# Kernel tuning notes

Hardware: AMD Instinct MI355X
Metric: run time of the kernel (lower is better)

The kernel has to match this reference:

```python
import jax, jax.numpy as jnp
import numpy as np

DIM = 64
N_EMBED = 1024
B, H, W = 64, 32, 32


def setup_inputs() -> dict:
    key = jax.random.key(0)
    k1, k2 = jax.random.split(key)
    inp = jax.random.normal(k1, (B, H, W, DIM), dtype=jnp.float32)
    embed = jax.random.normal(k2, (DIM, N_EMBED), dtype=jnp.float32)
    return {"input": inp, "embed": embed}


def reference(input, embed):
    # Eval-mode forward of Quantize (EMA buffer updates only run in training).
    dim, n_embed = embed.shape
    flat = input.reshape(-1, dim)  # [N, dim]
    dist = (jnp.sum(flat * flat, axis=1, keepdims=True)
            - 2.0 * (flat @ embed)
            + jnp.sum(embed * embed, axis=0, keepdims=True))
    embed_ind_flat = jnp.argmax(-dist, axis=1)  # nearest code per vector
    quantize_hard = jnp.take(embed.T, embed_ind_flat, axis=0).reshape(input.shape)
    # Soft (softmax-weighted) combine over the codebook
    quant = jax.nn.softmax(-dist, axis=-1) @ embed.T  # [N, dim]
    quant = quant.reshape(input.shape)
    embed_ind = embed_ind_flat.reshape(input.shape[:-1])
    diff = jnp.mean((jax.lax.stop_gradient(quantize_hard) - input) ** 2)
    # Straight-through: forward value = hard codes, gradient flows via soft quant
    quantize = quant + jax.lax.stop_gradient(quantize_hard - quant)
    embed_loss = jnp.mean((quantize - jax.lax.stop_gradient(input)) ** 2)
    return quantize, embed_ind, diff, embed_loss
```

## Files before the change

kernel.cpp:

```cpp
#include <hip/hip_runtime.h>
#include <math.h>

typedef __attribute__((ext_vector_type(8))) short short8;
typedef __attribute__((ext_vector_type(4))) float f32x4;
typedef unsigned short ushort_t;
typedef unsigned int uint_t;

#define DIM 64
#define NE 1024
#define NROW 65536
#define NELEM (NROW * DIM)
#define MARGIN 0.02f

#define OFF_BPACK 0
#define OFF_CN 262144
#define OFF_ET 266240
#define OFF_ACC 528384
#define OFF_FCNT 529408
#define OFF_DONE 529412
#define OFF_FLAGS 529424

__device__ __forceinline__ ushort_t f2bf(float f) {
  uint_t u = __float_as_uint(f);
  uint_t r = (u + 0x7FFFu + ((u >> 16) & 1u)) >> 16;
  return (ushort_t)r;
}

__global__ void prepack_kernel(const float* __restrict__ embed, ushort_t* __restrict__ bp,
                               float* __restrict__ cn, float* __restrict__ et,
                               double* __restrict__ acc, int* __restrict__ fcnt,
                               int* __restrict__ done) {
  __shared__ float nsum[8][32];
  const int tid = threadIdx.x;
  if (blockIdx.x == 0) {
    if (tid < 8) acc[tid * 16] = 0.0;
    if (tid == 0) {
      fcnt[0] = 0;
      done[0] = 0;
    }
  }
  const int cl_ = tid & 31;
  const int dg = tid >> 5;
  const int code = blockIdx.x * 32 + cl_;
  const int c16 = code >> 4, cl = code & 15;
  const int lane = cl + (dg & 3) * 16;
  const int kk = dg >> 2;

  float vals[8];
  float nrm = 0.f;
#pragma unroll
  for (int jd = 0; jd < 8; ++jd) {
    int d = dg * 8 + jd;
    float e = embed[d * NE + code];
    vals[jd] = e;
    nrm = fmaf(e, e, nrm);
  }
  nsum[dg][cl_] = nrm;

  float4 a = {vals[0], vals[1], vals[2], vals[3]};
  float4 b4 = {vals[4], vals[5], vals[6], vals[7]};
  *reinterpret_cast<float4*>(&et[(size_t)code * 64 + dg * 8]) = a;
  *reinterpret_cast<float4*>(&et[(size_t)code * 64 + dg * 8 + 4]) = b4;

  short8 hv, lv;
#pragma unroll
  for (int jd = 0; jd < 8; ++jd) {
    ushort_t h = f2bf(vals[jd]);
    float hf = __uint_as_float((uint_t)h << 16);
    hv[jd] = (short)h;
    lv[jd] = (short)f2bf(vals[jd] - hf);
  }
  *reinterpret_cast<short8*>(&bp[((size_t)(c16 * 4 + kk) * 64 + lane) * 8]) = hv;
  *reinterpret_cast<short8*>(&bp[((size_t)(c16 * 4 + 2 + kk) * 64 + lane) * 8]) = lv;

  __syncthreads();
  if (tid < 32) {
    float s = 0.f;
#pragma unroll
    for (int w = 0; w < 8; ++w) s += nsum[w][tid];
    cn[blockIdx.x * 32 + tid] = s;
  }
}

__launch_bounds__(64, 2)
__global__ void score_kernel(const float* __restrict__ input, const ushort_t* __restrict__ bp,
                             const float* __restrict__ cn, const float* __restrict__ et,
                             float* __restrict__ out, double* __restrict__ acc,
                             int* __restrict__ fcnt, int* __restrict__ flags) {
  __shared__ float cns[NE];
  const int lane = threadIdx.x;
  const int col = lane & 15, g = lane >> 4;
  const long rowbase = (long)blockIdx.x * 32;

#pragma unroll
  for (int i = 0; i < 4; ++i) {
    int o = i * 256 + lane * 4;
    *reinterpret_cast<float4*>(&cns[o]) = *reinterpret_cast<const float4*>(&cn[o]);
  }

  short8 ah[2][2], al[2][2];
#pragma unroll
  for (int rt = 0; rt < 2; ++rt)
#pragma unroll
    for (int kk = 0; kk < 2; ++kk) {
      const float* xp = &input[(size_t)(rowbase + rt * 16 + col) * 64 + kk * 32 + g * 8];
      float4 x0 = *reinterpret_cast<const float4*>(xp);
      float4 x1 = *reinterpret_cast<const float4*>(xp + 4);
      float xs[8] = {x0.x, x0.y, x0.z, x0.w, x1.x, x1.y, x1.z, x1.w};
#pragma unroll
      for (int j = 0; j < 8; ++j) {
        ushort_t h = f2bf(xs[j]);
        ah[rt][kk][j] = (short)h;
        float hf = __uint_as_float((uint_t)h << 16);
        al[rt][kk][j] = (short)f2bf(xs[j] - hf);
      }
    }

  float v1[2][4], v2[2][4];
  int i1[2][4];
#pragma unroll
  for (int rt = 0; rt < 2; ++rt)
#pragma unroll
    for (int r = 0; r < 4; ++r) {
      v1[rt][r] = -INFINITY;
      v2[rt][r] = -INFINITY;
      i1[rt][r] = 0;
    }

  __syncthreads();

  const short8* bpv = reinterpret_cast<const short8*>(bp);

  short8 b0h0, b0h1, b0l0, b0l1, b1h0, b1h1, b1l0, b1l1;
#define LOADB(B, cc)                       \
  {                                        \
    b##B##h0 = bpv[(cc)*256 + lane];       \
    b##B##h1 = bpv[(cc)*256 + 64 + lane];  \
    b##B##l0 = bpv[(cc)*256 + 128 + lane]; \
    b##B##l1 = bpv[(cc)*256 + 192 + lane]; \
  }

#define COMPUTE(B, cc)                                                            \
  {                                                                               \
    float cnv = cns[(cc)*16 + col];                                               \
    f32x4 aA = {0.f, 0.f, 0.f, 0.f};                                              \
    f32x4 aB = {0.f, 0.f, 0.f, 0.f};                                              \
    aA = __builtin_amdgcn_mfma_f32_16x16x32_bf16(ah[0][0], b##B##h0, aA, 0, 0, 0); \
    aB = __builtin_amdgcn_mfma_f32_16x16x32_bf16(ah[1][0], b##B##h0, aB, 0, 0, 0); \
    aA = __builtin_amdgcn_mfma_f32_16x16x32_bf16(ah[0][1], b##B##h1, aA, 0, 0, 0); \
    aB = __builtin_amdgcn_mfma_f32_16x16x32_bf16(ah[1][1], b##B##h1, aB, 0, 0, 0); \
    aA = __builtin_amdgcn_mfma_f32_16x16x32_bf16(al[0][0], b##B##h0, aA, 0, 0, 0); \
    aB = __builtin_amdgcn_mfma_f32_16x16x32_bf16(al[1][0], b##B##h0, aB, 0, 0, 0); \
    aA = __builtin_amdgcn_mfma_f32_16x16x32_bf16(al[0][1], b##B##h1, aA, 0, 0, 0); \
    aB = __builtin_amdgcn_mfma_f32_16x16x32_bf16(al[1][1], b##B##h1, aB, 0, 0, 0); \
    aA = __builtin_amdgcn_mfma_f32_16x16x32_bf16(ah[0][0], b##B##l0, aA, 0, 0, 0); \
    aB = __builtin_amdgcn_mfma_f32_16x16x32_bf16(ah[1][0], b##B##l0, aB, 0, 0, 0); \
    aA = __builtin_amdgcn_mfma_f32_16x16x32_bf16(ah[0][1], b##B##l1, aA, 0, 0, 0); \
    aB = __builtin_amdgcn_mfma_f32_16x16x32_bf16(ah[1][1], b##B##l1, aB, 0, 0, 0); \
    aA = __builtin_amdgcn_mfma_f32_16x16x32_bf16(al[0][0], b##B##l0, aA, 0, 0, 0); \
    aB = __builtin_amdgcn_mfma_f32_16x16x32_bf16(al[1][0], b##B##l0, aB, 0, 0, 0); \
    aA = __builtin_amdgcn_mfma_f32_16x16x32_bf16(al[0][1], b##B##l1, aA, 0, 0, 0); \
    aB = __builtin_amdgcn_mfma_f32_16x16x32_bf16(al[1][1], b##B##l1, aB, 0, 0, 0); \
    const int code = (cc)*16 + col;                                               \
    _Pragma("unroll") for (int r = 0; r < 4; ++r) {                               \
      float v = fmaf(2.f, aA[r], -cnv);                                           \
      v2[0][r] = __builtin_amdgcn_fmed3f(v, v1[0][r], v2[0][r]);                  \
      bool gt = v > v1[0][r];                                                     \
      i1[0][r] = gt ? code : i1[0][r];                                            \
      v1[0][r] = fmaxf(v1[0][r], v);                                              \
    }                                                                             \
    _Pragma("unroll") for (int r = 0; r < 4; ++r) {                               \
      float v = fmaf(2.f, aB[r], -cnv);                                           \
      v2[1][r] = __builtin_amdgcn_fmed3f(v, v1[1][r], v2[1][r]);                  \
      bool gt = v > v1[1][r];                                                     \
      i1[1][r] = gt ? code : i1[1][r];                                            \
      v1[1][r] = fmaxf(v1[1][r], v);                                              \
    }                                                                             \
  }

  LOADB(0, 0);
  LOADB(1, 1);
#pragma unroll 1
  for (int c = 0; c < 64; c += 2) {
    COMPUTE(0, c);
    if (c + 2 < 64) LOADB(0, c + 2);
    COMPUTE(1, c + 1);
    if (c + 3 < 64) LOADB(1, c + 3);
  }
#undef LOADB
#undef COMPUTE

  double lsum = 0.0;
#pragma unroll
  for (int rt = 0; rt < 2; ++rt)
#pragma unroll
    for (int r = 0; r < 4; ++r) {
      float bv1 = v1[rt][r], bv2 = v2[rt][r];
      int bidx = i1[rt][r];
#pragma unroll
      for (int off = 1; off <= 8; off <<= 1) {
        float ov1 = __shfl_xor(bv1, off);
        int oi = __shfl_xor(bidx, off);
        float ov2 = __shfl_xor(bv2, off);
        bool take = (ov1 > bv1) || (ov1 == bv1 && oi < bidx);
        float nv2 = take ? fmaxf(bv1, ov2) : fmaxf(bv2, ov1);
        bv1 = take ? ov1 : bv1;
        bidx = take ? oi : bidx;
        bv2 = nv2;
      }
      long row = rowbase + rt * 16 + g * 4 + r;
      float4 h = *reinterpret_cast<const float4*>(&et[(size_t)bidx * 64 + col * 4]);
      float4 x = *reinterpret_cast<const float4*>(&input[(size_t)row * 64 + col * 4]);
      *reinterpret_cast<float4*>(&out[(size_t)row * 64 + col * 4]) = h;
      float d0 = h.x - x.x, d1 = h.y - x.y, d2 = h.z - x.z, d3 = h.w - x.w;
      lsum += (double)(d0 * d0 + d1 * d1 + d2 * d2 + d3 * d3);
      if (col == 0) {
        out[NELEM + row] = (float)bidx;
        if (bv1 - bv2 < MARGIN) {
          int p = atomicAdd(fcnt, 1);
          flags[p] = (int)row;
        }
      }
    }

#pragma unroll
  for (int off = 1; off <= 32; off <<= 1) lsum += __shfl_xor(lsum, off);
  if (lane == 0) unsafeAtomicAdd(&acc[(blockIdx.x & 7) * 16], lsum);
}

__global__ void fixup_kernel(const float* __restrict__ input, const float* __restrict__ embed,
                             const float* __restrict__ et, float* __restrict__ out,
                             double* __restrict__ acc, const int* __restrict__ fcnt,
                             const int* __restrict__ flags, int* __restrict__ done) {
  __shared__ float Xs[8][64];
  __shared__ double Wv[4][8];
  __shared__ int Wi[4][8];
  __shared__ int NewI[8], OldI[8], Rw[8];
  const int tid = threadIdx.x;
  const int lane = tid & 63, wv = tid >> 6;
  const int count = *fcnt;

  for (int base = blockIdx.x * 8; base < count; base += gridDim.x * 8) {
    __syncthreads();
    if (tid < 8) {
      int p = base + tid;
      int r = (p < count) ? flags[p] : flags[count - 1];
      Rw[tid] = r;
      OldI[tid] = (int)out[NELEM + r];
    }
    __syncthreads();
    if (tid < 128) {
      int r8 = tid >> 4, seg = (tid & 15) * 4;
      *reinterpret_cast<float4*>(&Xs[r8][seg]) =
          *reinterpret_cast<const float4*>(&input[(size_t)Rw[r8] * 64 + seg]);
    }
    __syncthreads();

    const int j0 = tid * 4;
    double dot[8][4];
    double nrm[4];
#pragma unroll
    for (int r = 0; r < 8; ++r)
#pragma unroll
      for (int cc = 0; cc < 4; ++cc) dot[r][cc] = 0.0;
#pragma unroll
    for (int cc = 0; cc < 4; ++cc) nrm[cc] = 0.0;

#pragma unroll 1
    for (int d = 0; d < 64; d += 4) {
      float4 e4[4];
#pragma unroll
      for (int q = 0; q < 4; ++q)
        e4[q] = *reinterpret_cast<const float4*>(&embed[(d + q) * NE + j0]);
#pragma unroll
      for (int q = 0; q < 4; ++q) {
        double ev[4] = {(double)e4[q].x, (double)e4[q].y, (double)e4[q].z, (double)e4[q].w};
#pragma unroll
        for (int cc = 0; cc < 4; ++cc) nrm[cc] = fma(ev[cc], ev[cc], nrm[cc]);
#pragma unroll
        for (int r = 0; r < 8; ++r) {
          double xr = (double)Xs[r][d + q];
#pragma unroll
          for (int cc = 0; cc < 4; ++cc) dot[r][cc] = fma(xr, ev[cc], dot[r][cc]);
        }
      }
    }

#pragma unroll
    for (int r = 0; r < 8; ++r) {
      double bv = -1e300;
      int bi = 0;
#pragma unroll
      for (int cc = 0; cc < 4; ++cc) {
        double t = 2.0 * dot[r][cc] - nrm[cc];
        if (t > bv) {
          bv = t;
          bi = j0 + cc;
        }
      }
#pragma unroll
      for (int off = 1; off <= 32; off <<= 1) {
        double ob = __shfl_xor(bv, off);
        int oi = __shfl_xor(bi, off);
        if (ob > bv || (ob == bv && oi < bi)) {
          bv = ob;
          bi = oi;
        }
      }
      if (lane == 0) {
        Wv[wv][r] = bv;
        Wi[wv][r] = bi;
      }
    }
    __syncthreads();
    if (tid < 8) {
      double bv = Wv[0][tid];
      int bi = Wi[0][tid];
#pragma unroll
      for (int w = 1; w < 4; ++w) {
        double ob = Wv[w][tid];
        int oi = Wi[w][tid];
        if (ob > bv || (ob == bv && oi < bi)) {
          bv = ob;
          bi = oi;
        }
      }
      NewI[tid] = bi;
      if (base + tid < count && bi != OldI[tid]) out[NELEM + Rw[tid]] = (float)bi;
    }
    __syncthreads();
    if (tid < 128) {
      int r8 = tid >> 4, seg = (tid & 15) * 4;
      if (base + r8 < count && NewI[r8] != OldI[r8]) {
        float4 hn = *reinterpret_cast<const float4*>(&et[(size_t)NewI[r8] * 64 + seg]);
        float4 ho = *reinterpret_cast<const float4*>(&et[(size_t)OldI[r8] * 64 + seg]);
        float4 x = *reinterpret_cast<const float4*>(&Xs[r8][seg]);
        *reinterpret_cast<float4*>(&out[(size_t)Rw[r8] * 64 + seg]) = hn;
        float n0 = hn.x - x.x, n1 = hn.y - x.y, n2 = hn.z - x.z, n3 = hn.w - x.w;
        float o0 = ho.x - x.x, o1 = ho.y - x.y, o2 = ho.z - x.z, o3 = ho.w - x.w;
        double delta = (double)(n0 * n0 + n1 * n1 + n2 * n2 + n3 * n3) -
                       (double)(o0 * o0 + o1 * o1 + o2 * o2 + o3 * o3);
        unsafeAtomicAdd(&acc[(blockIdx.x & 7) * 16], delta);
      }
    }
  }

  __syncthreads();
  if (tid == 0) {
    __threadfence();
    int prev = atomicAdd(done, 1);
    if (prev == (int)gridDim.x - 1) {
      double v = 0.0;
#pragma unroll
      for (int w = 0; w < 8; ++w) v += unsafeAtomicAdd(&acc[w * 16], 0.0);
      float f = (float)(v / (double)NELEM);
      out[NELEM + NROW + 0] = f;
      out[NELEM + NROW + 1] = f;
    }
  }
}

extern "C" void kernel_launch(void* const* d_in, const int* in_sizes, int n_in,
                              void* d_out, int out_size, void* d_ws, size_t ws_size,
                              hipStream_t stream) {
  const float* input = (const float*)d_in[0];
  const float* embed = (const float*)d_in[1];
  float* out = (float*)d_out;
  char* ws = (char*)d_ws;
  ushort_t* bp = (ushort_t*)(ws + OFF_BPACK);
  float* cn = (float*)(ws + OFF_CN);
  float* et = (float*)(ws + OFF_ET);
  double* acc = (double*)(ws + OFF_ACC);
  int* fcnt = (int*)(ws + OFF_FCNT);
  int* done = (int*)(ws + OFF_DONE);
  int* flags = (int*)(ws + OFF_FLAGS);

  prepack_kernel<<<32, 256, 0, stream>>>(embed, bp, cn, et, acc, fcnt, done);
  score_kernel<<<NROW / 32, 64, 0, stream>>>(input, bp, cn, et, out, acc, fcnt, flags);
  fixup_kernel<<<256, 256, 0, stream>>>(input, embed, et, out, acc, fcnt, flags, done);
}
```

Measured before the change: 138.3 us.

## Fuse fixup pass into score kernel and drop low-low MFMA term

Removes the separate fixup kernel. Rows whose top-two score margin is small are now rechecked in double precision inside the score kernel, using a wave-wide ballot loop over a transposed codebook copy. The MFMA product drops the lo*lo bf16 term, uses two independent accumulator chains, and triple-buffers the codebook loads. The prepack kernel is reshaped to 64-thread blocks that reduce norms with shuffles. This removes a kernel launch and the global flag list, at the cost of serialized double-precision work in blocks that contain ambiguous rows.

```diff
diff --git a/kernel.cpp b/kernel.cpp
--- a/kernel.cpp
+++ b/kernel.cpp
@@ -2,6 +2,7 @@
 #include <math.h>
 
 typedef __attribute__((ext_vector_type(8))) short short8;
+typedef __attribute__((ext_vector_type(4))) short short4v;
 typedef __attribute__((ext_vector_type(4))) float f32x4;
 typedef unsigned short ushort_t;
 typedef unsigned int uint_t;
@@ -11,14 +12,13 @@
 #define NROW 65536
 #define NELEM (NROW * DIM)
 #define MARGIN 0.02f
+#define NBLK 2048
 
 #define OFF_BPACK 0
 #define OFF_CN 262144
 #define OFF_ET 266240
 #define OFF_ACC 528384
-#define OFF_FCNT 529408
-#define OFF_DONE 529412
-#define OFF_FLAGS 529424
+#define OFF_DONE 529408
 
 __device__ __forceinline__ ushort_t f2bf(float f) {
   uint_t u = __float_as_uint(f);
@@ -28,66 +28,52 @@
 
 __global__ void prepack_kernel(const float* __restrict__ embed, ushort_t* __restrict__ bp,
                                float* __restrict__ cn, float* __restrict__ et,
-                               double* __restrict__ acc, int* __restrict__ fcnt,
-                               int* __restrict__ done) {
-  __shared__ float nsum[8][32];
-  const int tid = threadIdx.x;
-  if (blockIdx.x == 0) {
-    if (tid < 8) acc[tid * 16] = 0.0;
-    if (tid == 0) {
-      fcnt[0] = 0;
-      done[0] = 0;
-    }
-  }
-  const int cl_ = tid & 31;
-  const int dg = tid >> 5;
-  const int code = blockIdx.x * 32 + cl_;
+                               double* __restrict__ acc, int* __restrict__ done) {
+  const int lane = threadIdx.x;
+  const int blk = blockIdx.x;
+  if (blk == 0) {
+    if (lane < 8) acc[lane * 16] = 0.0;
+    if (lane == 8) done[0] = 0;
+  }
+  const int code = blk * 4 + (lane >> 4);
+  const int dg = lane & 15;
+  const int d0 = dg * 4;
+  float e[4];
+  float nrm = 0.f;
+#pragma unroll
+  for (int q = 0; q < 4; ++q) {
+    e[q] = embed[(d0 + q) * NE + code];
+    nrm = fmaf(e[q], e[q], nrm);
+  }
+  float4 ev = {e[0], e[1], e[2], e[3]};
+  *reinterpret_cast<float4*>(&et[(size_t)code * 64 + d0]) = ev;
+
+  short4v hv, lv;
+#pragma unroll
+  for (int q = 0; q < 4; ++q) {
+    ushort_t h = f2bf(e[q]);
+    float hf = __uint_as_float((uint_t)h << 16);
+    hv[q] = (short)h;
+    lv[q] = (short)f2bf(e[q] - hf);
+  }
   const int c16 = code >> 4, cl = code & 15;
-  const int lane = cl + (dg & 3) * 16;
-  const int kk = dg >> 2;
-
-  float vals[8];
-  float nrm = 0.f;
-#pragma unroll
-  for (int jd = 0; jd < 8; ++jd) {
-    int d = dg * 8 + jd;
-    float e = embed[d * NE + code];
-    vals[jd] = e;
-    nrm = fmaf(e, e, nrm);
-  }
-  nsum[dg][cl_] = nrm;
-
-  float4 a = {vals[0], vals[1], vals[2], vals[3]};
-  float4 b4 = {vals[4], vals[5], vals[6], vals[7]};
-  *reinterpret_cast<float4*>(&et[(size_t)code * 64 + dg * 8]) = a;
-  *reinterpret_cast<float4*>(&et[(size_t)code * 64 + dg * 8 + 4]) = b4;
-
-  short8 hv, lv;
-#pragma unroll
-  for (int jd = 0; jd < 8; ++jd) {
-    ushort_t h = f2bf(vals[jd]);
-    float hf = __uint_as_float((uint_t)h << 16);
-    hv[jd] = (short)h;
-    lv[jd] = (short)f2bf(vals[jd] - hf);
-  }
-  *reinterpret_cast<short8*>(&bp[((size_t)(c16 * 4 + kk) * 64 + lane) * 8]) = hv;
-  *reinterpret_cast<short8*>(&bp[((size_t)(c16 * 4 + 2 + kk) * 64 + lane) * 8]) = lv;
-
-  __syncthreads();
-  if (tid < 32) {
-    float s = 0.f;
-#pragma unroll
-    for (int w = 0; w < 8; ++w) s += nsum[w][tid];
-    cn[blockIdx.x * 32 + tid] = s;
-  }
+  const int lane16 = cl + ((d0 >> 3) & 3) * 16;
+  const int kk = d0 >> 5;
+  const int j0 = d0 & 7;
+  *reinterpret_cast<short4v*>(&bp[((size_t)(c16 * 4 + kk) * 64 + lane16) * 8 + j0]) = hv;
+  *reinterpret_cast<short4v*>(&bp[((size_t)(c16 * 4 + 2 + kk) * 64 + lane16) * 8 + j0]) = lv;
+
+#pragma unroll
+  for (int off = 1; off <= 8; off <<= 1) nrm += __shfl_xor(nrm, off);
+  if (dg == 0) cn[code] = nrm;
 }
 
 __launch_bounds__(64, 2)
 __global__ void score_kernel(const float* __restrict__ input, const ushort_t* __restrict__ bp,
                              const float* __restrict__ cn, const float* __restrict__ et,
                              float* __restrict__ out, double* __restrict__ acc,
-                             int* __restrict__ fcnt, int* __restrict__ flags) {
-  __shared__ float cns[NE];
+                             int* __restrict__ done) {
+  __shared__ __align__(16) float cns[NE];
   const int lane = threadIdx.x;
   const int col = lane & 15, g = lane >> 4;
   const long rowbase = (long)blockIdx.x * 32;
@@ -130,8 +116,8 @@
   __syncthreads();
 
   const short8* bpv = reinterpret_cast<const short8*>(bp);
-
-  short8 b0h0, b0h1, b0l0, b0l1, b1h0, b1h1, b1l0, b1l1;
+  short8 b0h0, b0h1, b0l0, b0l1, b1h0, b1h1, b1l0, b1l1, b2h0, b2h1, b2l0, b2l1;
+
 #define LOADB(B, cc)                       \
   {                                        \
     b##B##h0 = bpv[(cc)*256 + lane];       \
@@ -140,57 +126,58 @@
     b##B##l1 = bpv[(cc)*256 + 192 + lane]; \
   }
 
-#define COMPUTE(B, cc)                                                            \
-  {                                                                               \
-    float cnv = cns[(cc)*16 + col];                                               \
-    f32x4 aA = {0.f, 0.f, 0.f, 0.f};                                              \
-    f32x4 aB = {0.f, 0.f, 0.f, 0.f};                                              \
-    aA = __builtin_amdgcn_mfma_f32_16x16x32_bf16(ah[0][0], b##B##h0, aA, 0, 0, 0); \
-    aB = __builtin_amdgcn_mfma_f32_16x16x32_bf16(ah[1][0], b##B##h0, aB, 0, 0, 0); \
-    aA = __builtin_amdgcn_mfma_f32_16x16x32_bf16(ah[0][1], b##B##h1, aA, 0, 0, 0); \
-    aB = __builtin_amdgcn_mfma_f32_16x16x32_bf16(ah[1][1], b##B##h1, aB, 0, 0, 0); \
-    aA = __builtin_amdgcn_mfma_f32_16x16x32_bf16(al[0][0], b##B##h0, aA, 0, 0, 0); \
-    aB = __builtin_amdgcn_mfma_f32_16x16x32_bf16(al[1][0], b##B##h0, aB, 0, 0, 0); \
-    aA = __builtin_amdgcn_mfma_f32_16x16x32_bf16(al[0][1], b##B##h1, aA, 0, 0, 0); \
-    aB = __builtin_amdgcn_mfma_f32_16x16x32_bf16(al[1][1], b##B##h1, aB, 0, 0, 0); \
-    aA = __builtin_amdgcn_mfma_f32_16x16x32_bf16(ah[0][0], b##B##l0, aA, 0, 0, 0); \
-    aB = __builtin_amdgcn_mfma_f32_16x16x32_bf16(ah[1][0], b##B##l0, aB, 0, 0, 0); \
-    aA = __builtin_amdgcn_mfma_f32_16x16x32_bf16(ah[0][1], b##B##l1, aA, 0, 0, 0); \
-    aB = __builtin_amdgcn_mfma_f32_16x16x32_bf16(ah[1][1], b##B##l1, aB, 0, 0, 0); \
-    aA = __builtin_amdgcn_mfma_f32_16x16x32_bf16(al[0][0], b##B##l0, aA, 0, 0, 0); \
-    aB = __builtin_amdgcn_mfma_f32_16x16x32_bf16(al[1][0], b##B##l0, aB, 0, 0, 0); \
-    aA = __builtin_amdgcn_mfma_f32_16x16x32_bf16(al[0][1], b##B##l1, aA, 0, 0, 0); \
-    aB = __builtin_amdgcn_mfma_f32_16x16x32_bf16(al[1][1], b##B##l1, aB, 0, 0, 0); \
-    const int code = (cc)*16 + col;                                               \
-    _Pragma("unroll") for (int r = 0; r < 4; ++r) {                               \
-      float v = fmaf(2.f, aA[r], -cnv);                                           \
-      v2[0][r] = __builtin_amdgcn_fmed3f(v, v1[0][r], v2[0][r]);                  \
-      bool gt = v > v1[0][r];                                                     \
-      i1[0][r] = gt ? code : i1[0][r];                                            \
-      v1[0][r] = fmaxf(v1[0][r], v);                                              \
-    }                                                                             \
-    _Pragma("unroll") for (int r = 0; r < 4; ++r) {                               \
-      float v = fmaf(2.f, aB[r], -cnv);                                           \
-      v2[1][r] = __builtin_amdgcn_fmed3f(v, v1[1][r], v2[1][r]);                  \
-      bool gt = v > v1[1][r];                                                     \
-      i1[1][r] = gt ? code : i1[1][r];                                            \
-      v1[1][r] = fmaxf(v1[1][r], v);                                              \
-    }                                                                             \
+#define COMPUTE(B, cc)                                                             \
+  {                                                                                \
+    float cnv = cns[(cc)*16 + col];                                                \
+    f32x4 uA = {0.f, 0.f, 0.f, 0.f};                                               \
+    f32x4 uB = {0.f, 0.f, 0.f, 0.f};                                               \
+    f32x4 vA = {0.f, 0.f, 0.f, 0.f};                                               \
+    f32x4 vB = {0.f, 0.f, 0.f, 0.f};                                               \
+    uA = __builtin_amdgcn_mfma_f32_16x16x32_bf16(ah[0][0], b##B##h0, uA, 0, 0, 0); \
+    uB = __builtin_amdgcn_mfma_f32_16x16x32_bf16(ah[1][0], b##B##h0, uB, 0, 0, 0); \
+    vA = __builtin_amdgcn_mfma_f32_16x16x32_bf16(ah[0][0], b##B##l0, vA, 0, 0, 0); \
+    vB = __builtin_amdgcn_mfma_f32_16x16x32_bf16(ah[1][0], b##B##l0, vB, 0, 0, 0); \
+    uA = __builtin_amdgcn_mfma_f32_16x16x32_bf16(ah[0][1], b##B##h1, uA, 0, 0, 0); \
+    uB = __builtin_amdgcn_mfma_f32_16x16x32_bf16(ah[1][1], b##B##h1, uB, 0, 0, 0); \
+    vA = __builtin_amdgcn_mfma_f32_16x16x32_bf16(ah[0][1], b##B##l1, vA, 0, 0, 0); \
+    vB = __builtin_amdgcn_mfma_f32_16x16x32_bf16(ah[1][1], b##B##l1, vB, 0, 0, 0); \
+    vA = __builtin_amdgcn_mfma_f32_16x16x32_bf16(al[0][0], b##B##h0, vA, 0, 0, 0); \
+    vB = __builtin_amdgcn_mfma_f32_16x16x32_bf16(al[1][0], b##B##h0, vB, 0, 0, 0); \
+    vA = __builtin_amdgcn_mfma_f32_16x16x32_bf16(al[0][1], b##B##h1, vA, 0, 0, 0); \
+    vB = __builtin_amdgcn_mfma_f32_16x16x32_bf16(al[1][1], b##B##h1, vB, 0, 0, 0); \
+    const int code = (cc)*16 + col;                                                \
+    _Pragma("unroll") for (int r = 0; r < 4; ++r) {                                \
+      float v = fmaf(2.f, uA[r] + vA[r], -cnv);                                    \
+      v2[0][r] = __builtin_amdgcn_fmed3f(v, v1[0][r], v2[0][r]);                   \
+      bool gt = v > v1[0][r];                                                      \
+      i1[0][r] = gt ? code : i1[0][r];                                             \
+      v1[0][r] = fmaxf(v1[0][r], v);                                               \
+    }                                                                              \
+    _Pragma("unroll") for (int r = 0; r < 4; ++r) {                                \
+      float v = fmaf(2.f, uB[r] + vB[r], -cnv);                                    \
+      v2[1][r] = __builtin_amdgcn_fmed3f(v, v1[1][r], v2[1][r]);                   \
+      bool gt = v > v1[1][r];                                                      \
+      i1[1][r] = gt ? code : i1[1][r];                                             \
+      v1[1][r] = fmaxf(v1[1][r], v);                                               \
+    }                                                                              \
   }
 
   LOADB(0, 0);
   LOADB(1, 1);
+  LOADB(2, 2);
 #pragma unroll 1
-  for (int c = 0; c < 64; c += 2) {
+  for (int c = 0; c < 63; c += 3) {
     COMPUTE(0, c);
-    if (c + 2 < 64) LOADB(0, c + 2);
+    if (c + 3 < 64) LOADB(0, c + 3);
     COMPUTE(1, c + 1);
-    if (c + 3 < 64) LOADB(1, c + 3);
-  }
+    if (c + 4 < 64) LOADB(1, c + 4);
+    COMPUTE(2, c + 2);
+    if (c + 5 < 64) LOADB(2, c + 5);
+  }
+  COMPUTE(0, 63);
 #undef LOADB
 #undef COMPUTE
 
-  double lsum = 0.0;
 #pragma unroll
   for (int rt = 0; rt < 2; ++rt)
 #pragma unroll
@@ -208,148 +195,85 @@
         bidx = take ? oi : bidx;
         bv2 = nv2;
       }
-      long row = rowbase + rt * 16 + g * 4 + r;
+      v1[rt][r] = bv1;
+      v2[rt][r] = bv2;
+      i1[rt][r] = bidx;
+    }
+
+#pragma unroll
+  for (int rt = 0; rt < 2; ++rt)
+#pragma unroll
+    for (int r = 0; r < 4; ++r) {
+      unsigned long long m = __ballot(col == 0 && (v1[rt][r] - v2[rt][r] < MARGIN));
+      while (m) {
+        int p = __ffsll((unsigned long long)m) - 1;
+        m &= m - 1;
+        const int gg = p >> 4;
+        const long row = rowbase + rt * 16 + gg * 4 + r;
+        __syncthreads();
+        cns[lane] = input[(size_t)row * 64 + lane];
+        __syncthreads();
+        double bt = -1e300;
+        int bj = 0;
+#pragma unroll 1
+        for (int jj = 0; jj < 16; ++jj) {
+          const int j = lane * 16 + jj;
+          double dot = 0.0, nr = 0.0;
+#pragma unroll 4
+          for (int d = 0; d < 64; d += 4) {
+            float4 evv = *reinterpret_cast<const float4*>(&et[(size_t)j * 64 + d]);
+            float4 xv = *reinterpret_cast<const float4*>(&cns[d]);
+            dot = fma((double)xv.x, (double)evv.x, dot);
+            nr = fma((double)evv.x, (double)evv.x, nr);
+            dot = fma((double)xv.y, (double)evv.y, dot);
+            nr = fma((double)evv.y, (double)evv.y, nr);
+            dot = fma((double)xv.z, (double)evv.z, dot);
+            nr = fma((double)evv.z, (double)evv.z, nr);
+            dot = fma((double)xv.w, (double)evv.w, dot);
+            nr = fma((double)evv.w, (double)evv.w, nr);
+          }
+          double t = 2.0 * dot - nr;
+          if (t > bt) {
+            bt = t;
+            bj = j;
+          }
+        }
+#pragma unroll
+        for (int off = 1; off <= 32; off <<= 1) {
+          double ot = __shfl_xor(bt, off);
+          int oj = __shfl_xor(bj, off);
+          if (ot > bt || (ot == bt && oj < bj)) {
+            bt = ot;
+            bj = oj;
+          }
+        }
+        if (g == gg) i1[rt][r] = bj;
+      }
+    }
+
+  double lsum = 0.0;
+#pragma unroll
+  for (int rt = 0; rt < 2; ++rt)
+#pragma unroll
+    for (int r = 0; r < 4; ++r) {
+      const int bidx = i1[rt][r];
+      const long row = rowbase + rt * 16 + g * 4 + r;
       float4 h = *reinterpret_cast<const float4*>(&et[(size_t)bidx * 64 + col * 4]);
       float4 x = *reinterpret_cast<const float4*>(&input[(size_t)row * 64 + col * 4]);
       *reinterpret_cast<float4*>(&out[(size_t)row * 64 + col * 4]) = h;
       float d0 = h.x - x.x, d1 = h.y - x.y, d2 = h.z - x.z, d3 = h.w - x.w;
       lsum += (double)(d0 * d0 + d1 * d1 + d2 * d2 + d3 * d3);
-      if (col == 0) {
-        out[NELEM + row] = (float)bidx;
-        if (bv1 - bv2 < MARGIN) {
-          int p = atomicAdd(fcnt, 1);
-          flags[p] = (int)row;
-        }
-      }
-    }
-
+      if (col == 0) out[NELEM + row] = (float)bidx;
+    }
 #pragma unroll
   for (int off = 1; off <= 32; off <<= 1) lsum += __shfl_xor(lsum, off);
-  if (lane == 0) unsafeAtomicAdd(&acc[(blockIdx.x & 7) * 16], lsum);
-}
-
-__global__ void fixup_kernel(const float* __restrict__ input, const float* __restrict__ embed,
-                             const float* __restrict__ et, float* __restrict__ out,
-                             double* __restrict__ acc, const int* __restrict__ fcnt,
-                             const int* __restrict__ flags, int* __restrict__ done) {
-  __shared__ float Xs[8][64];
-  __shared__ double Wv[4][8];
-  __shared__ int Wi[4][8];
-  __shared__ int NewI[8], OldI[8], Rw[8];
-  const int tid = threadIdx.x;
-  const int lane = tid & 63, wv = tid >> 6;
-  const int count = *fcnt;
-
-  for (int base = blockIdx.x * 8; base < count; base += gridDim.x * 8) {
-    __syncthreads();
-    if (tid < 8) {
-      int p = base + tid;
-      int r = (p < count) ? flags[p] : flags[count - 1];
-      Rw[tid] = r;
-      OldI[tid] = (int)out[NELEM + r];
-    }
-    __syncthreads();
-    if (tid < 128) {
-      int r8 = tid >> 4, seg = (tid & 15) * 4;
-      *reinterpret_cast<float4*>(&Xs[r8][seg]) =
-          *reinterpret_cast<const float4*>(&input[(size_t)Rw[r8] * 64 + seg]);
-    }
-    __syncthreads();
-
-    const int j0 = tid * 4;
-    double dot[8][4];
-    double nrm[4];
-#pragma unroll
-    for (int r = 0; r < 8; ++r)
-#pragma unroll
-      for (int cc = 0; cc < 4; ++cc) dot[r][cc] = 0.0;
-#pragma unroll
-    for (int cc = 0; cc < 4; ++cc) nrm[cc] = 0.0;
-
-#pragma unroll 1
-    for (int d = 0; d < 64; d += 4) {
-      float4 e4[4];
-#pragma unroll
-      for (int q = 0; q < 4; ++q)
-        e4[q] = *reinterpret_cast<const float4*>(&embed[(d + q) * NE + j0]);
-#pragma unroll
-      for (int q = 0; q < 4; ++q) {
-        double ev[4] = {(double)e4[q].x, (double)e4[q].y, (double)e4[q].z, (double)e4[q].w};
-#pragma unroll
-        for (int cc = 0; cc < 4; ++cc) nrm[cc] = fma(ev[cc], ev[cc], nrm[cc]);
-#pragma unroll
-        for (int r = 0; r < 8; ++r) {
-          double xr = (double)Xs[r][d + q];
-#pragma unroll
-          for (int cc = 0; cc < 4; ++cc) dot[r][cc] = fma(xr, ev[cc], dot[r][cc]);
-        }
-      }
-    }
-
-#pragma unroll
-    for (int r = 0; r < 8; ++r) {
-      double bv = -1e300;
-      int bi = 0;
-#pragma unroll
-      for (int cc = 0; cc < 4; ++cc) {
-        double t = 2.0 * dot[r][cc] - nrm[cc];
-        if (t > bv) {
-          bv = t;
-          bi = j0 + cc;
-        }
-      }
-#pragma unroll
-      for (int off = 1; off <= 32; off <<= 1) {
-        double ob = __shfl_xor(bv, off);
-        int oi = __shfl_xor(bi, off);
-        if (ob > bv || (ob == bv && oi < bi)) {
-          bv = ob;
-          bi = oi;
-        }
-      }
-      if (lane == 0) {
-        Wv[wv][r] = bv;
-        Wi[wv][r] = bi;
-      }
-    }
-    __syncthreads();
-    if (tid < 8) {
-      double bv = Wv[0][tid];
-      int bi = Wi[0][tid];
-#pragma unroll
-      for (int w = 1; w < 4; ++w) {
-        double ob = Wv[w][tid];
-        int oi = Wi[w][tid];
-        if (ob > bv || (ob == bv && oi < bi)) {
-          bv = ob;
-          bi = oi;
-        }
-      }
-      NewI[tid] = bi;
-      if (base + tid < count && bi != OldI[tid]) out[NELEM + Rw[tid]] = (float)bi;
-    }
-    __syncthreads();
-    if (tid < 128) {
-      int r8 = tid >> 4, seg = (tid & 15) * 4;
-      if (base + r8 < count && NewI[r8] != OldI[r8]) {
-        float4 hn = *reinterpret_cast<const float4*>(&et[(size_t)NewI[r8] * 64 + seg]);
-        float4 ho = *reinterpret_cast<const float4*>(&et[(size_t)OldI[r8] * 64 + seg]);
-        float4 x = *reinterpret_cast<const float4*>(&Xs[r8][seg]);
-        *reinterpret_cast<float4*>(&out[(size_t)Rw[r8] * 64 + seg]) = hn;
-        float n0 = hn.x - x.x, n1 = hn.y - x.y, n2 = hn.z - x.z, n3 = hn.w - x.w;
-        float o0 = ho.x - x.x, o1 = ho.y - x.y, o2 = ho.z - x.z, o3 = ho.w - x.w;
-        double delta = (double)(n0 * n0 + n1 * n1 + n2 * n2 + n3 * n3) -
-                       (double)(o0 * o0 + o1 * o1 + o2 * o2 + o3 * o3);
-        unsafeAtomicAdd(&acc[(blockIdx.x & 7) * 16], delta);
-      }
-    }
-  }
-
-  __syncthreads();
-  if (tid == 0) {
-    __threadfence();
+  if (lane == 0) unsafeAtomicAdd(&acc[((int)blockIdx.x & 7) * 16], lsum);
+
+  __threadfence();
+  if (lane == 0) {
     int prev = atomicAdd(done, 1);
     if (prev == (int)gridDim.x - 1) {
+      __threadfence();
       double v = 0.0;
 #pragma unroll
       for (int w = 0; w < 8; ++w) v += unsafeAtomicAdd(&acc[w * 16], 0.0);
@@ -371,11 +295,8 @@
   float* cn = (float*)(ws + OFF_CN);
   float* et = (float*)(ws + OFF_ET);
   double* acc = (double*)(ws + OFF_ACC);
-  int* fcnt = (int*)(ws + OFF_FCNT);
   int* done = (int*)(ws + OFF_DONE);
-  int* flags = (int*)(ws + OFF_FLAGS);
-
-  prepack_kernel<<<32, 256, 0, stream>>>(embed, bp, cn, et, acc, fcnt, done);
-  score_kernel<<<NROW / 32, 64, 0, stream>>>(input, bp, cn, et, out, acc, fcnt, flags);
-  fixup_kernel<<<256, 256, 0, stream>>>(input, embed, et, out, acc, fcnt, flags, done);
+
+  prepack_kernel<<<256, 64, 0, stream>>>(embed, bp, cn, et, acc, done);
+  score_kernel<<<NBLK, 64, 0, stream>>>(input, bp, cn, et, out, acc, done);
 }
```

Result: slower. 235.9 us (+70.5%).
